# Performance work log

Hardware: AMD Instinct MI355X
Metric: run time of the kernel (lower is better)

Reference implementation:

```python
import jax, jax.numpy as jnp
import numpy as np

# dims
B, N, NF, NEF = 32, 256, 3, 3          # batch, nodes, node feats, edge feats
D, FF, H, L = 768, 3072, 12, 6         # embed, ffn, heads, layers
NA, ND, NE, NS = 512, 512, 512, 512    # vocab sizes (atoms, degrees, edges, spatial)
S = N + 1                              # +1 graph token
HD = D // H
SCALE = HD ** -0.5
EPS = 1e-5


def setup_inputs() -> dict:
    key = jax.random.key(0)
    ki = iter(jax.random.split(key, 64))
    def nrm(shape, std):
        return jax.random.normal(next(ki), shape, jnp.float32) * std
    lin_std = 0.02 / np.sqrt(L)
    inp = {}
    inp['x'] = jax.random.randint(next(ki), (B, N, NF), 0, NA)
    inp['attn_bias'] = jnp.zeros((B, S, S), jnp.float32)
    inp['spatial_pos'] = jax.random.randint(next(ki), (B, N, N), 0, NS)
    inp['attn_edge_type'] = jax.random.randint(next(ki), (B, N, N, NEF), 0, NE)
    inp['in_degree'] = jax.random.randint(next(ki), (B, N), 0, ND)
    inp['out_degree'] = jax.random.randint(next(ki), (B, N), 0, ND)
    # embedding tables (init_params overwrites padding rows with normals, so no zero row)
    inp['atom_emb'] = nrm((NA + 1, D), 0.02)
    inp['in_deg_emb'] = nrm((ND, D), 0.02)
    inp['out_deg_emb'] = nrm((ND, D), 0.02)
    inp['graph_token'] = nrm((1, D), 0.02)
    inp['spatial_emb'] = nrm((NS, H), 0.02)
    inp['edge_emb'] = nrm((NE + 1, H), 0.02)
    inp['virt_dist'] = nrm((1, H), 0.02)
    # stacked per-layer params (torch Linear convention: W is [out,in])
    for nm in ('Wq', 'Wk', 'Wv', 'Wo'):
        inp[nm] = nrm((L, D, D), lin_std)
    for nm in ('bq', 'bk', 'bv', 'bo'):
        inp[nm] = jnp.zeros((L, D), jnp.float32)
    inp['ln1_g'] = jnp.ones((L, D), jnp.float32); inp['ln1_b'] = jnp.zeros((L, D), jnp.float32)
    inp['ln2_g'] = jnp.ones((L, D), jnp.float32); inp['ln2_b'] = jnp.zeros((L, D), jnp.float32)
    inp['W1'] = nrm((L, FF, D), lin_std); inp['b1'] = jnp.zeros((L, FF), jnp.float32)
    inp['W2'] = nrm((L, D, FF), lin_std); inp['b2'] = jnp.zeros((L, D), jnp.float32)
    inp['fin_g'] = jnp.ones((D,), jnp.float32); inp['fin_b'] = jnp.zeros((D,), jnp.float32)
    return inp


def _ln(x, g, b):
    m = x.mean(-1, keepdims=True)
    v = jnp.mean((x - m) ** 2, axis=-1, keepdims=True)
    return (x - m) * jax.lax.rsqrt(v + EPS) * g + b


def _forward(x, attn_bias, spatial_pos, attn_edge_type, in_degree, out_degree, P):
    # --- GraphNodeFeature ---
    nf = P['atom_emb'][jnp.clip(x, 0, NA)].sum(-2)                     # [B,N,D]
    nf = nf + P['in_deg_emb'][jnp.clip(in_degree, 0, ND - 1)]
    nf = nf + P['out_deg_emb'][jnp.clip(out_degree, 0, ND - 1)]
    h = jnp.concatenate([jnp.broadcast_to(P['graph_token'][None], (B, 1, D)), nf], axis=1)  # [B,S,D]
    # --- GraphAttnBias ---
    inner = (P['spatial_emb'][jnp.clip(spatial_pos, 0, NS - 1)]
             + P['edge_emb'][jnp.clip(attn_edge_type, 0, NE)].mean(-2))  # [B,N,N,H]
    gb = jnp.broadcast_to(attn_bias[:, None], (B, H, S, S))
    gb = gb.at[:, :, 1:, 1:].add(jnp.transpose(inner, (0, 3, 1, 2)))
    t = P['virt_dist'].reshape(1, H, 1)
    gb = gb.at[:, :, 1:, 0].add(t)
    gb = gb.at[:, :, 0, :].add(t)
    # key padding mask: node is padded iff first feature index == 0; graph token never padded
    pad = jnp.concatenate([jnp.zeros((B, 1), bool), x[:, :, 0] == 0], axis=1)  # [B,S]
    maskk = pad[:, None, None, :]

    def step(hh, p):
        Wq, bq, Wk, bk, Wv, bv, Wo, bo, g1, bb_g1, W1, bf1, W2, bf2, g2, bb_g2 = p
        # pre-LN self-attention
        z = _ln(hh, g1, bb_g1)
        q = (jnp.einsum('bsi,oi->bso', z, Wq) + bq) * SCALE
        k = jnp.einsum('bsi,oi->bso', z, Wk) + bk
        v = jnp.einsum('bsi,oi->bso', z, Wv) + bv
        q = q.reshape(B, S, H, HD); k = k.reshape(B, S, H, HD); v = v.reshape(B, S, H, HD)
        scores = jnp.einsum('bqhd,bkhd->bhqk', q, k) + gb
        scores = jnp.where(maskk, -jnp.inf, scores)
        a = jax.nn.softmax(scores, axis=-1)
        o = jnp.einsum('bhqk,bkhd->bqhd', a, v).reshape(B, S, D)
        hh = hh + jnp.einsum('bsi,oi->bso', o, Wo) + bo
        # pre-LN FFN
        z = _ln(hh, g2, bb_g2)
        f = jax.nn.gelu(jnp.einsum('bsi,oi->bso', z, W1) + bf1, approximate=False)
        hh = hh + jnp.einsum('bsi,oi->bso', f, W2) + bf2
        return hh, None

    layer_params = (P['Wq'], P['bq'], P['Wk'], P['bk'], P['Wv'], P['bv'], P['Wo'], P['bo'],
                    P['ln1_g'], P['ln1_b'], P['W1'], P['b1'], P['W2'], P['b2'], P['ln2_g'], P['ln2_b'])
    h, _ = jax.lax.scan(step, h, layer_params)
    h = _ln(h, P['fin_g'], P['fin_b'])
    return h  # [B,S,D]


def reference(x, attn_bias, spatial_pos, attn_edge_type, in_degree, out_degree,
              atom_emb, in_deg_emb, out_deg_emb, graph_token, spatial_emb, edge_emb, virt_dist,
              Wq, Wk, Wv, Wo, bq, bk, bv, bo, ln1_g, ln1_b, ln2_g, ln2_b,
              W1, b1, W2, b2, fin_g, fin_b):
    P = dict(atom_emb=atom_emb, in_deg_emb=in_deg_emb, out_deg_emb=out_deg_emb,
             graph_token=graph_token, spatial_emb=spatial_emb, edge_emb=edge_emb, virt_dist=virt_dist,
             Wq=Wq, Wk=Wk, Wv=Wv, Wo=Wo, bq=bq, bk=bk, bv=bv, bo=bo,
             ln1_g=ln1_g, ln1_b=ln1_b, ln2_g=ln2_g, ln2_b=ln2_b,
             W1=W1, b1=b1, W2=W2, b2=b2, fin_g=fin_g, fin_b=fin_b)
    h = _forward(x, attn_bias, spatial_pos, attn_edge_type, in_degree, out_degree, P)
    node_rep = h[:, 1:, :]   # [B,N,D]
    graph_rep = h[:, 0, :]   # [B,D]
    return node_rep, graph_rep
```

## Files before the change

kernel.cpp:

```cpp
#include <hip/hip_runtime.h>
#include <hip/hip_bf16.h>
#include <math.h>

#define B_   32
#define N_   256
#define S_   257
#define D_   768
#define FF_  3072
#define H_   12
#define HD_  64
#define L_   6
#define NA_  512
#define ND_  512
#define NE_  512
#define NS_  512
#define SCALE_ 0.125f
#define EPS_ 1e-5f
#define NEG_BIG_ (-1e30f)

#define DD_  (D_ * D_)
#define FD_  (FF_ * D_)
#define WTOT_ (4 * DD_ + 2 * FD_)

typedef __hip_bfloat16 bf16;
typedef __attribute__((ext_vector_type(8))) short bf16x8;
typedef __attribute__((ext_vector_type(4))) float f32x4;

#define AS1 __attribute__((address_space(1)))
#define AS3 __attribute__((address_space(3)))

static __device__ __forceinline__ int iclamp(int v, int lo, int hi) {
    return v < lo ? lo : (v > hi ? hi : v);
}
static __device__ __forceinline__ float b2f(bf16 v) { return (float)v; }
static __device__ __forceinline__ short f2b(float f) {
    union { bf16 b; short s; } u; u.b = __float2bfloat16(f); return u.s;
}

__global__ __launch_bounds__(256) void embed_kernel(
    const int* __restrict__ x, const int* __restrict__ indeg,
    const int* __restrict__ outdeg, const float* __restrict__ atom_emb,
    const float* __restrict__ ine, const float* __restrict__ oute,
    const float* __restrict__ gtok, float* __restrict__ h)
{
    int row = blockIdx.x;
    int b = row / S_, s = row % S_;
    int t = threadIdx.x;
    float* hr = h + (size_t)row * D_;
    if (s == 0) {
        for (int d = t; d < D_; d += 256) hr[d] = gtok[d];
        return;
    }
    int n = s - 1;
    size_t xb = ((size_t)b * N_ + n) * 3;
    int i0 = iclamp(x[xb + 0], 0, NA_);
    int i1 = iclamp(x[xb + 1], 0, NA_);
    int i2 = iclamp(x[xb + 2], 0, NA_);
    int id = iclamp(indeg[(size_t)b * N_ + n], 0, ND_ - 1);
    int od = iclamp(outdeg[(size_t)b * N_ + n], 0, ND_ - 1);
    const float* a0 = atom_emb + (size_t)i0 * D_;
    const float* a1 = atom_emb + (size_t)i1 * D_;
    const float* a2 = atom_emb + (size_t)i2 * D_;
    const float* pi = ine + (size_t)id * D_;
    const float* po = oute + (size_t)od * D_;
    for (int d = t; d < D_; d += 256)
        hr[d] = a0[d] + a1[d] + a2[d] + pi[d] + po[d];
}

__global__ __launch_bounds__(256) void bias_kernel(
    const int* __restrict__ x, const float* __restrict__ ab,
    const int* __restrict__ sp, const int* __restrict__ et,
    const float* __restrict__ spemb, const float* __restrict__ eemb,
    const float* __restrict__ virt, bf16* __restrict__ bias)
{
    int row = blockIdx.x;
    int b = row / S_, q = row % S_;
    for (int k = threadIdx.x; k < S_; k += 256) {
        float abv = ab[((size_t)b * S_ + q) * S_ + k];
        bool masked = (k >= 1) && (x[((size_t)b * N_ + (k - 1)) * 3] == 0);
        size_t out_base = (size_t)b * H_ * S_ * S_ + (size_t)q * S_ + k;
        if (masked) {
            #pragma unroll
            for (int hh = 0; hh < H_; hh++)
                bias[out_base + (size_t)hh * S_ * S_] = __float2bfloat16(NEG_BIG_);
        } else if (q == 0 || k == 0) {
            #pragma unroll
            for (int hh = 0; hh < H_; hh++)
                bias[out_base + (size_t)hh * S_ * S_] = __float2bfloat16(abv + virt[hh]);
        } else {
            int spv = iclamp(sp[((size_t)b * N_ + (q - 1)) * N_ + (k - 1)], 0, NS_ - 1);
            size_t eb = (((size_t)b * N_ + (q - 1)) * N_ + (k - 1)) * 3;
            int e0 = iclamp(et[eb + 0], 0, NE_);
            int e1 = iclamp(et[eb + 1], 0, NE_);
            int e2 = iclamp(et[eb + 2], 0, NE_);
            #pragma unroll
            for (int hh = 0; hh < H_; hh++) {
                float inner = spemb[spv * H_ + hh]
                    + (eemb[e0 * H_ + hh] + eemb[e1 * H_ + hh] + eemb[e2 * H_ + hh]) * (1.0f / 3.0f);
                bias[out_base + (size_t)hh * S_ * S_] = __float2bfloat16(abv + inner);
            }
        }
    }
}

__global__ __launch_bounds__(256) void cvt_w_kernel(
    const float* __restrict__ Wq, const float* __restrict__ Wk,
    const float* __restrict__ Wv, const float* __restrict__ Wo,
    const float* __restrict__ W1, const float* __restrict__ W2,
    int layer, bf16* __restrict__ dst)
{
    size_t i = ((size_t)blockIdx.x * 256 + threadIdx.x) * 8;
    if (i >= (size_t)WTOT_) return;
    const float* src;
    if (i < (size_t)4 * DD_) {
        size_t r = i / DD_;
        const float* base = (r == 0) ? Wq : (r == 1) ? Wk : (r == 2) ? Wv : Wo;
        src = base + (size_t)layer * DD_ + (i - r * DD_);
    } else if (i < (size_t)4 * DD_ + FD_) {
        src = W1 + (size_t)layer * FD_ + (i - (size_t)4 * DD_);
    } else {
        src = W2 + (size_t)layer * FD_ + (i - (size_t)4 * DD_ - FD_);
    }
    float4 a = *(const float4*)src;
    float4 c = *(const float4*)(src + 4);
    *(bf16x8*)((short*)dst + i) =
        (bf16x8){f2b(a.x), f2b(a.y), f2b(a.z), f2b(a.w),
                 f2b(c.x), f2b(c.y), f2b(c.z), f2b(c.w)};
}

__global__ __launch_bounds__(256) void ln_kernel(
    const float* __restrict__ x, bf16* __restrict__ y,
    const float* __restrict__ g, const float* __restrict__ b)
{
    int row = blockIdx.x;
    int t = threadIdx.x;
    const float* xr = x + (size_t)row * D_;
    bf16* yr = y + (size_t)row * D_;
    float v0 = xr[t], v1 = xr[t + 256], v2 = xr[t + 512];
    __shared__ float rs[256], rq[256];
    rs[t] = v0 + v1 + v2;
    rq[t] = v0 * v0 + v1 * v1 + v2 * v2;
    __syncthreads();
    for (int o = 128; o > 0; o >>= 1) {
        if (t < o) { rs[t] += rs[t + o]; rq[t] += rq[t + o]; }
        __syncthreads();
    }
    float mean = rs[0] * (1.0f / D_);
    float var = fmaxf(rq[0] * (1.0f / D_) - mean * mean, 0.f);
    float inv = rsqrtf(var + EPS_);
    yr[t]       = __float2bfloat16((v0 - mean) * inv * g[t]       + b[t]);
    yr[t + 256] = __float2bfloat16((v1 - mean) * inv * g[t + 256] + b[t + 256]);
    yr[t + 512] = __float2bfloat16((v2 - mean) * inv * g[t + 512] + b[t + 512]);
}

__global__ __launch_bounds__(256) void final_ln_kernel(
    const float* __restrict__ x, const float* __restrict__ g,
    const float* __restrict__ b, float* __restrict__ out)
{
    int row = blockIdx.x;
    int bb = row / S_, s = row % S_;
    int t = threadIdx.x;
    const float* xr = x + (size_t)row * D_;
    float v0 = xr[t], v1 = xr[t + 256], v2 = xr[t + 512];
    __shared__ float rs[256], rq[256];
    rs[t] = v0 + v1 + v2;
    rq[t] = v0 * v0 + v1 * v1 + v2 * v2;
    __syncthreads();
    for (int o = 128; o > 0; o >>= 1) {
        if (t < o) { rs[t] += rs[t + o]; rq[t] += rq[t + o]; }
        __syncthreads();
    }
    float mean = rs[0] * (1.0f / D_);
    float var = fmaxf(rq[0] * (1.0f / D_) - mean * mean, 0.f);
    float inv = rsqrtf(var + EPS_);
    float* dst = (s == 0) ? out + (size_t)B_ * N_ * D_ + (size_t)bb * D_
                          : out + ((size_t)bb * N_ + (s - 1)) * D_;
    dst[t]       = (v0 - mean) * inv * g[t]       + b[t];
    dst[t + 256] = (v1 - mean) * inv * g[t + 256] + b[t + 256];
    dst[t + 512] = (v2 - mean) * inv * g[t + 512] + b[t + 512];
}

template <typename TC, int MODE>
__global__ __launch_bounds__(256) void mgemm(
    const bf16* __restrict__ A, const bf16* __restrict__ W,
    const float* __restrict__ bias, const float* __restrict__ res,
    TC* __restrict__ C, int M, int N, int K, float scale)
{
    __shared__ short As[128 * 32];
    __shared__ short Ws[128 * 32];
    AS3 short* AsL = (AS3 short*)As;
    AS3 short* WsL = (AS3 short*)Ws;
    const int t = threadIdx.x;
    const int lane = t & 63;
    const int w = t >> 6;
    const int wm = w & 1, wn = w >> 1;
    const int quad = lane >> 4;
    const int col = lane & 15;
    const int block_m = blockIdx.x * 128;
    const int block_n = blockIdx.y * 128;

    const int lrow = lane >> 2;
    const int lcol = (lane & 3) * 8;

    f32x4 acc[4][4];
    #pragma unroll
    for (int i = 0; i < 4; i++)
        #pragma unroll
        for (int j = 0; j < 4; j++)
            acc[i][j] = (f32x4){0.f, 0.f, 0.f, 0.f};

    for (int k0 = 0; k0 < K; k0 += 32) {
        #pragma unroll
        for (int ss = 0; ss < 2; ss++) {
            int seg = w * 2 + ss;
            int row = seg * 16 + lrow;
            const bf16* ga = A + (size_t)(block_m + row) * K + k0 + lcol;
            __builtin_amdgcn_global_load_lds((const AS1 void*)ga,
                                             (AS3 void*)(AsL + seg * 512), 16, 0, 0);
            const bf16* gw = W + (size_t)(block_n + row) * K + k0 + lcol;
            __builtin_amdgcn_global_load_lds((const AS1 void*)gw,
                                             (AS3 void*)(WsL + seg * 512), 16, 0, 0);
        }
        __syncthreads();
        bf16x8 af[4], bfr[4];
        #pragma unroll
        for (int mt = 0; mt < 4; mt++)
            af[mt] = *(const bf16x8*)&As[(wm * 64 + mt * 16 + col) * 32 + quad * 8];
        #pragma unroll
        for (int nt = 0; nt < 4; nt++)
            bfr[nt] = *(const bf16x8*)&Ws[(wn * 64 + nt * 16 + col) * 32 + quad * 8];
        #pragma unroll
        for (int mt = 0; mt < 4; mt++)
            #pragma unroll
            for (int nt = 0; nt < 4; nt++)
                acc[mt][nt] = __builtin_amdgcn_mfma_f32_16x16x32_bf16(
                    af[mt], bfr[nt], acc[mt][nt], 0, 0, 0);
        __syncthreads();
    }

    #pragma unroll
    for (int mt = 0; mt < 4; mt++) {
        #pragma unroll
        for (int nt = 0; nt < 4; nt++) {
            int gn = block_n + wn * 64 + nt * 16 + col;
            float bn = bias[gn];
            #pragma unroll
            for (int r = 0; r < 4; r++) {
                int gm = block_m + wm * 64 + mt * 16 + quad * 4 + r;
                if (gm < M) {
                    float val = acc[mt][nt][r] + bn;
                    if (MODE == 1) val *= scale;
                    if (MODE == 2) val = 0.5f * val * (1.0f + erff(val * 0.70710678118654752f));
                    if (MODE == 3) val += res[(size_t)gm * N + gn];
                    C[(size_t)gm * N + gn] = (TC)val;
                }
            }
        }
    }
}

__global__ __launch_bounds__(256) void attn_mfma(
    const bf16* __restrict__ qb, const bf16* __restrict__ kb,
    const bf16* __restrict__ vb, const bf16* __restrict__ bias,
    bf16* __restrict__ ob)
{
    __shared__ short Ks[64 * 72];
    __shared__ short Vt[64 * 72];
    __shared__ short Ps[4][16 * 72];

    const int t = threadIdx.x;
    const int lane = t & 63;
    const int wq = t >> 6;
    const int quad = lane >> 4;
    const int col = lane & 15;
    const int bh = blockIdx.y;
    const int hh = bh % H_;
    const int b = bh / H_;
    const int q0 = blockIdx.x * 64;

    bf16x8 qf[2];
    {
        int qrow = q0 + wq * 16 + col;
        #pragma unroll
        for (int kk = 0; kk < 2; kk++) {
            bf16x8 v = (bf16x8){0, 0, 0, 0, 0, 0, 0, 0};
            if (qrow < S_)
                v = *(const bf16x8*)(qb + ((size_t)(b * S_ + qrow)) * D_ + hh * HD_ + kk * 32 + quad * 8);
            qf[kk] = v;
        }
    }

    f32x4 o_acc[4];
    #pragma unroll
    for (int nt = 0; nt < 4; nt++) o_acc[nt] = (f32x4){0.f, 0.f, 0.f, 0.f};
    float m_run[4], l_run[4];
    #pragma unroll
    for (int r = 0; r < 4; r++) { m_run[r] = NEG_BIG_; l_run[r] = 0.f; }

    for (int kc = 0; kc < 5; kc++) {
        const int kbase = kc * 64;
        #pragma unroll
        for (int ss = 0; ss < 2; ss++) {
            int s = t + ss * 256;
            int row = s >> 3, dg = (s & 7) * 8;
            int gk = kbase + row;
            bf16x8 v = (bf16x8){0, 0, 0, 0, 0, 0, 0, 0};
            if (gk < S_)
                v = *(const bf16x8*)(kb + ((size_t)(b * S_ + gk)) * D_ + hh * HD_ + dg);
            *(bf16x8*)&Ks[row * 72 + dg] = v;
        }
        {
            int d = wq * 16 + col;
            const bf16* vcol = vb + ((size_t)(b * S_)) * D_ + hh * HD_ + d;
            #pragma unroll
            for (int ss = 0; ss < 8; ss++) {
                int kp = ss * 4 + quad;
                int gk = kbase + kp * 2;
                short v0 = (gk     < S_) ? *(const short*)(vcol + (size_t)gk * D_)       : (short)0;
                short v1 = (gk + 1 < S_) ? *(const short*)(vcol + (size_t)(gk + 1) * D_) : (short)0;
                unsigned pk = ((unsigned)(unsigned short)v0) |
                              ((unsigned)(unsigned short)v1 << 16);
                *(unsigned*)&Vt[d * 72 + kp * 2] = pk;
            }
        }
        __syncthreads();

        f32x4 s_acc[4];
        #pragma unroll
        for (int nt = 0; nt < 4; nt++) s_acc[nt] = (f32x4){0.f, 0.f, 0.f, 0.f};
        #pragma unroll
        for (int nt = 0; nt < 4; nt++) {
            #pragma unroll
            for (int kk = 0; kk < 2; kk++) {
                bf16x8 kfrag = *(const bf16x8*)&Ks[(nt * 16 + col) * 72 + kk * 32 + quad * 8];
                s_acc[nt] = __builtin_amdgcn_mfma_f32_16x16x32_bf16(qf[kk], kfrag, s_acc[nt], 0, 0, 0);
            }
        }

        const int qrow_base = q0 + wq * 16 + quad * 4;
        #pragma unroll
        for (int nt = 0; nt < 4; nt++) {
            int kglob = kbase + nt * 16 + col;
            #pragma unroll
            for (int r = 0; r < 4; r++) {
                int q = qrow_base + r;
                float sv = s_acc[nt][r];
                if (kglob >= S_)       sv = NEG_BIG_;
                else if (q < S_)       sv += b2f(bias[((size_t)bh * S_ + q) * S_ + kglob]);
                s_acc[nt][r] = sv;
            }
        }

        float alpha[4];
        #pragma unroll
        for (int r = 0; r < 4; r++) {
            float mx = fmaxf(fmaxf(s_acc[0][r], s_acc[1][r]),
                             fmaxf(s_acc[2][r], s_acc[3][r]));
            #pragma unroll
            for (int off = 8; off; off >>= 1) mx = fmaxf(mx, __shfl_xor(mx, off));
            float m_new = fmaxf(m_run[r], mx);
            alpha[r] = __expf(m_run[r] - m_new);
            m_run[r] = m_new;
            float ps = 0.f;
            #pragma unroll
            for (int nt = 0; nt < 4; nt++) {
                float p = __expf(s_acc[nt][r] - m_new);
                s_acc[nt][r] = p;
                ps += p;
            }
            #pragma unroll
            for (int off = 8; off; off >>= 1) ps += __shfl_xor(ps, off);
            l_run[r] = l_run[r] * alpha[r] + ps;
        }

        #pragma unroll
        for (int nt = 0; nt < 4; nt++)
            #pragma unroll
            for (int r = 0; r < 4; r++)
                Ps[wq][(quad * 4 + r) * 72 + nt * 16 + col] = f2b(s_acc[nt][r]);
        #pragma unroll
        for (int nt = 0; nt < 4; nt++)
            #pragma unroll
            for (int r = 0; r < 4; r++)
                o_acc[nt][r] *= alpha[r];

        bf16x8 pf[2];
        pf[0] = *(const bf16x8*)&Ps[wq][col * 72 + quad * 8];
        pf[1] = *(const bf16x8*)&Ps[wq][col * 72 + 32 + quad * 8];
        #pragma unroll
        for (int nt = 0; nt < 4; nt++) {
            #pragma unroll
            for (int kk = 0; kk < 2; kk++) {
                bf16x8 vfrag = *(const bf16x8*)&Vt[(nt * 16 + col) * 72 + kk * 32 + quad * 8];
                o_acc[nt] = __builtin_amdgcn_mfma_f32_16x16x32_bf16(pf[kk], vfrag, o_acc[nt], 0, 0, 0);
            }
        }
        __syncthreads();
    }

    const int qrow_base = q0 + wq * 16 + quad * 4;
    #pragma unroll
    for (int r = 0; r < 4; r++) {
        int q = qrow_base + r;
        if (q >= S_) continue;
        float invl = 1.0f / l_run[r];
        bf16* orow = ob + ((size_t)(b * S_ + q)) * D_ + hh * HD_;
        #pragma unroll
        for (int nt = 0; nt < 4; nt++)
            orow[nt * 16 + col] = __float2bfloat16(o_acc[nt][r] * invl);
    }
}

extern "C" void kernel_launch(void* const* d_in, const int* in_sizes, int n_in,
                              void* d_out, int out_size, void* d_ws, size_t ws_size,
                              hipStream_t stream)
{
    const int*   x         = (const int*)d_in[0];
    const float* attn_bias = (const float*)d_in[1];
    const int*   spatial   = (const int*)d_in[2];
    const int*   edget     = (const int*)d_in[3];
    const int*   indeg     = (const int*)d_in[4];
    const int*   outdeg    = (const int*)d_in[5];
    const float* atom_emb  = (const float*)d_in[6];
    const float* ine       = (const float*)d_in[7];
    const float* oute      = (const float*)d_in[8];
    const float* gtok      = (const float*)d_in[9];
    const float* spemb     = (const float*)d_in[10];
    const float* eemb      = (const float*)d_in[11];
    const float* virt      = (const float*)d_in[12];
    const float* Wq        = (const float*)d_in[13];
    const float* Wk        = (const float*)d_in[14];
    const float* Wv        = (const float*)d_in[15];
    const float* Wo        = (const float*)d_in[16];
    const float* bq        = (const float*)d_in[17];
    const float* bk        = (const float*)d_in[18];
    const float* bvv       = (const float*)d_in[19];
    const float* bo        = (const float*)d_in[20];
    const float* ln1g      = (const float*)d_in[21];
    const float* ln1b      = (const float*)d_in[22];
    const float* ln2g      = (const float*)d_in[23];
    const float* ln2b      = (const float*)d_in[24];
    const float* W1        = (const float*)d_in[25];
    const float* b1        = (const float*)d_in[26];
    const float* W2        = (const float*)d_in[27];
    const float* b2        = (const float*)d_in[28];
    const float* fing      = (const float*)d_in[29];
    const float* finb      = (const float*)d_in[30];

    const int M = B_ * S_;
    char* wsp = (char*)d_ws;
    size_t off = 0;
    auto alloc = [&](size_t bytes) -> void* {
        void* p = (void*)(wsp + off);
        off += (bytes + 255) & ~(size_t)255;
        return p;
    };
    float* h    = (float*)alloc((size_t)M * D_ * 4);
    bf16*  z    = (bf16*)alloc((size_t)M * D_ * 2);
    bf16*  qkv  = (bf16*)alloc((size_t)M * FF_ * 2);
    bf16*  bias = (bf16*)alloc((size_t)B_ * H_ * S_ * S_ * 2);
    bf16*  wbf  = (bf16*)alloc((size_t)WTOT_ * 2);
    bf16* qbuf = qkv;
    bf16* kbuf = qkv + (size_t)M * D_;
    bf16* vbuf = qkv + (size_t)2 * M * D_;
    bf16* fbuf = qkv;
    bf16* obuf = z;

    embed_kernel<<<M, 256, 0, stream>>>(x, indeg, outdeg, atom_emb, ine, oute, gtok, h);
    bias_kernel<<<M, 256, 0, stream>>>(x, attn_bias, spatial, edget, spemb, eemb, virt, bias);

    dim3 gD((M + 127) / 128, D_ / 128);
    dim3 gF((M + 127) / 128, FF_ / 128);
    dim3 gA(5, B_ * H_);
    const int cvtBlocks = WTOT_ / 2048;

    for (int l = 0; l < L_; l++) {
        cvt_w_kernel<<<cvtBlocks, 256, 0, stream>>>(Wq, Wk, Wv, Wo, W1, W2, l, wbf);
        ln_kernel<<<M, 256, 0, stream>>>(h, z, ln1g + l * D_, ln1b + l * D_);
        mgemm<bf16, 1><<<gD, 256, 0, stream>>>(z, wbf,            bq + l * D_, nullptr, qbuf, M, D_, D_, SCALE_);
        mgemm<bf16, 0><<<gD, 256, 0, stream>>>(z, wbf + DD_,      bk + l * D_, nullptr, kbuf, M, D_, D_, 1.f);
        mgemm<bf16, 0><<<gD, 256, 0, stream>>>(z, wbf + 2 * DD_,  bvv + l * D_, nullptr, vbuf, M, D_, D_, 1.f);
        attn_mfma<<<gA, 256, 0, stream>>>(qbuf, kbuf, vbuf, bias, obuf);
        mgemm<float, 3><<<gD, 256, 0, stream>>>(obuf, wbf + 3 * DD_, bo + l * D_, h, h, M, D_, D_, 1.f);
        ln_kernel<<<M, 256, 0, stream>>>(h, z, ln2g + l * D_, ln2b + l * D_);
        mgemm<bf16, 2><<<gF, 256, 0, stream>>>(z, wbf + 4 * DD_, b1 + l * FF_, nullptr, fbuf, M, FF_, D_, 1.f);
        mgemm<float, 3><<<gD, 256, 0, stream>>>(fbuf, wbf + 4 * DD_ + FD_, b2 + l * D_, h, h, M, D_, FF_, 1.f);
    }
    final_ln_kernel<<<M, 256, 0, stream>>>(h, fing, finb, (float*)d_out);
}
```

Before: 2.857 ms.

## Fuse QKV projections, double-buffer GEMM LDS, and remap workgroups across XCDs

```diff
diff --git a/kernel.cpp b/kernel.cpp
--- a/kernel.cpp
+++ b/kernel.cpp
@@ -21,6 +21,7 @@
 #define DD_  (D_ * D_)
 #define FD_  (FF_ * D_)
 #define WTOT_ (4 * DD_ + 2 * FD_)
+#define QKVN_ 2304
 
 typedef __hip_bfloat16 bf16;
 typedef __attribute__((ext_vector_type(8))) short bf16x8;
@@ -112,10 +113,12 @@
     size_t i = ((size_t)blockIdx.x * 256 + threadIdx.x) * 8;
     if (i >= (size_t)WTOT_) return;
     const float* src;
+    float sc = 1.f;
     if (i < (size_t)4 * DD_) {
         size_t r = i / DD_;
         const float* base = (r == 0) ? Wq : (r == 1) ? Wk : (r == 2) ? Wv : Wo;
         src = base + (size_t)layer * DD_ + (i - r * DD_);
+        if (r == 0) sc = SCALE_;
     } else if (i < (size_t)4 * DD_ + FD_) {
         src = W1 + (size_t)layer * FD_ + (i - (size_t)4 * DD_);
     } else {
@@ -124,8 +127,21 @@
     float4 a = *(const float4*)src;
     float4 c = *(const float4*)(src + 4);
     *(bf16x8*)((short*)dst + i) =
-        (bf16x8){f2b(a.x), f2b(a.y), f2b(a.z), f2b(a.w),
-                 f2b(c.x), f2b(c.y), f2b(c.z), f2b(c.w)};
+        (bf16x8){f2b(a.x * sc), f2b(a.y * sc), f2b(a.z * sc), f2b(a.w * sc),
+                 f2b(c.x * sc), f2b(c.y * sc), f2b(c.z * sc), f2b(c.w * sc)};
+}
+
+__global__ __launch_bounds__(256) void pack_bias_kernel(
+    const float* __restrict__ bq, const float* __restrict__ bk,
+    const float* __restrict__ bv, int layer, float* __restrict__ bqkv)
+{
+    int i = blockIdx.x * 256 + threadIdx.x;
+    if (i >= QKVN_) return;
+    float v;
+    if (i < D_)            v = bq[layer * D_ + i] * SCALE_;
+    else if (i < 2 * D_)   v = bk[layer * D_ + (i - D_)];
+    else                   v = bv[layer * D_ + (i - 2 * D_)];
+    bqkv[i] = v;
 }
 
 __global__ __launch_bounds__(256) void ln_kernel(
@@ -184,72 +200,85 @@
 __global__ __launch_bounds__(256) void mgemm(
     const bf16* __restrict__ A, const bf16* __restrict__ W,
     const float* __restrict__ bias, const float* __restrict__ res,
-    TC* __restrict__ C, int M, int N, int K, float scale)
-{
-    __shared__ short As[128 * 32];
-    __shared__ short Ws[128 * 32];
-    AS3 short* AsL = (AS3 short*)As;
-    AS3 short* WsL = (AS3 short*)Ws;
+    TC* __restrict__ C, int M, int N, int K, int gx)
+{
+    __shared__ short As[2][128 * 32];
+    __shared__ short Ws[2][128 * 32];
+    AS3 short* AsL = (AS3 short*)&As[0][0];
+    AS3 short* WsL = (AS3 short*)&Ws[0][0];
     const int t = threadIdx.x;
     const int lane = t & 63;
     const int w = t >> 6;
     const int wm = w & 1, wn = w >> 1;
     const int quad = lane >> 4;
     const int col = lane & 15;
-    const int block_m = blockIdx.x * 128;
-    const int block_n = blockIdx.y * 128;
+
+    const int nwg = gridDim.x;
+    const int orig = blockIdx.x;
+    const int q8 = nwg >> 3, r8 = nwg & 7;
+    const int xcd = orig & 7, li = orig >> 3;
+    const int wgid = (xcd < r8 ? xcd * (q8 + 1) : r8 * (q8 + 1) + (xcd - r8) * q8) + li;
+    const int block_m = (wgid % gx) * 128;
+    const int block_n = (wgid / gx) * 128;
 
     const int lrow = lane >> 2;
     const int lcol = (lane & 3) * 8;
 
-    f32x4 acc[4][4];
-    #pragma unroll
-    for (int i = 0; i < 4; i++)
-        #pragma unroll
-        for (int j = 0; j < 4; j++)
-            acc[i][j] = (f32x4){0.f, 0.f, 0.f, 0.f};
-
-    for (int k0 = 0; k0 < K; k0 += 32) {
+    auto stage = [&](int buf, int k0) {
         #pragma unroll
         for (int ss = 0; ss < 2; ss++) {
             int seg = w * 2 + ss;
             int row = seg * 16 + lrow;
             const bf16* ga = A + (size_t)(block_m + row) * K + k0 + lcol;
             __builtin_amdgcn_global_load_lds((const AS1 void*)ga,
-                                             (AS3 void*)(AsL + seg * 512), 16, 0, 0);
+                (AS3 void*)(AsL + buf * (128 * 32) + seg * 512), 16, 0, 0);
             const bf16* gw = W + (size_t)(block_n + row) * K + k0 + lcol;
             __builtin_amdgcn_global_load_lds((const AS1 void*)gw,
-                                             (AS3 void*)(WsL + seg * 512), 16, 0, 0);
-        }
+                (AS3 void*)(WsL + buf * (128 * 32) + seg * 512), 16, 0, 0);
+        }
+    };
+
+    f32x4 acc[4][4];
+    #pragma unroll
+    for (int i = 0; i < 4; i++)
+        #pragma unroll
+        for (int j = 0; j < 4; j++)
+            acc[i][j] = (f32x4){0.f, 0.f, 0.f, 0.f};
+
+    const int nt = K >> 5;
+    stage(0, 0);
+    __syncthreads();
+    int cur = 0;
+    for (int tt = 0; tt < nt; tt++) {
+        if (tt + 1 < nt) stage(cur ^ 1, (tt + 1) << 5);
+        bf16x8 af[4], bfr[4];
+        #pragma unroll
+        for (int mt = 0; mt < 4; mt++)
+            af[mt] = *(const bf16x8*)&As[cur][(wm * 64 + mt * 16 + col) * 32 + quad * 8];
+        #pragma unroll
+        for (int ntt = 0; ntt < 4; ntt++)
+            bfr[ntt] = *(const bf16x8*)&Ws[cur][(wn * 64 + ntt * 16 + col) * 32 + quad * 8];
+        #pragma unroll
+        for (int mt = 0; mt < 4; mt++)
+            #pragma unroll
+            for (int ntt = 0; ntt < 4; ntt++)
+                acc[mt][ntt] = __builtin_amdgcn_mfma_f32_16x16x32_bf16(
+                    af[mt], bfr[ntt], acc[mt][ntt], 0, 0, 0);
         __syncthreads();
-        bf16x8 af[4], bfr[4];
-        #pragma unroll
-        for (int mt = 0; mt < 4; mt++)
-            af[mt] = *(const bf16x8*)&As[(wm * 64 + mt * 16 + col) * 32 + quad * 8];
-        #pragma unroll
-        for (int nt = 0; nt < 4; nt++)
-            bfr[nt] = *(const bf16x8*)&Ws[(wn * 64 + nt * 16 + col) * 32 + quad * 8];
-        #pragma unroll
-        for (int mt = 0; mt < 4; mt++)
-            #pragma unroll
-            for (int nt = 0; nt < 4; nt++)
-                acc[mt][nt] = __builtin_amdgcn_mfma_f32_16x16x32_bf16(
-                    af[mt], bfr[nt], acc[mt][nt], 0, 0, 0);
-        __syncthreads();
+        cur ^= 1;
     }
 
     #pragma unroll
     for (int mt = 0; mt < 4; mt++) {
         #pragma unroll
-        for (int nt = 0; nt < 4; nt++) {
-            int gn = block_n + wn * 64 + nt * 16 + col;
+        for (int ntt = 0; ntt < 4; ntt++) {
+            int gn = block_n + wn * 64 + ntt * 16 + col;
             float bn = bias[gn];
             #pragma unroll
             for (int r = 0; r < 4; r++) {
                 int gm = block_m + wm * 64 + mt * 16 + quad * 4 + r;
                 if (gm < M) {
-                    float val = acc[mt][nt][r] + bn;
-                    if (MODE == 1) val *= scale;
+                    float val = acc[mt][ntt][r] + bn;
                     if (MODE == 2) val = 0.5f * val * (1.0f + erff(val * 0.70710678118654752f));
                     if (MODE == 3) val += res[(size_t)gm * N + gn];
                     C[(size_t)gm * N + gn] = (TC)val;
@@ -260,10 +289,12 @@
 }
 
 __global__ __launch_bounds__(256) void attn_mfma(
-    const bf16* __restrict__ qb, const bf16* __restrict__ kb,
-    const bf16* __restrict__ vb, const bf16* __restrict__ bias,
+    const bf16* __restrict__ qkv, const bf16* __restrict__ bias,
     bf16* __restrict__ ob)
 {
+    const bf16* qb = qkv;
+    const bf16* kb = qkv + D_;
+    const bf16* vb = qkv + 2 * D_;
     __shared__ short Ks[64 * 72];
     __shared__ short Vt[64 * 72];
     __shared__ short Ps[4][16 * 72];
@@ -285,7 +316,7 @@
         for (int kk = 0; kk < 2; kk++) {
             bf16x8 v = (bf16x8){0, 0, 0, 0, 0, 0, 0, 0};
             if (qrow < S_)
-                v = *(const bf16x8*)(qb + ((size_t)(b * S_ + qrow)) * D_ + hh * HD_ + kk * 32 + quad * 8);
+                v = *(const bf16x8*)(qb + ((size_t)(b * S_ + qrow)) * QKVN_ + hh * HD_ + kk * 32 + quad * 8);
             qf[kk] = v;
         }
     }
@@ -306,18 +337,18 @@
             int gk = kbase + row;
             bf16x8 v = (bf16x8){0, 0, 0, 0, 0, 0, 0, 0};
             if (gk < S_)
-                v = *(const bf16x8*)(kb + ((size_t)(b * S_ + gk)) * D_ + hh * HD_ + dg);
+                v = *(const bf16x8*)(kb + ((size_t)(b * S_ + gk)) * QKVN_ + hh * HD_ + dg);
             *(bf16x8*)&Ks[row * 72 + dg] = v;
         }
         {
             int d = wq * 16 + col;
-            const bf16* vcol = vb + ((size_t)(b * S_)) * D_ + hh * HD_ + d;
+            const bf16* vcol = vb + ((size_t)(b * S_)) * QKVN_ + hh * HD_ + d;
             #pragma unroll
             for (int ss = 0; ss < 8; ss++) {
                 int kp = ss * 4 + quad;
                 int gk = kbase + kp * 2;
-                short v0 = (gk     < S_) ? *(const short*)(vcol + (size_t)gk * D_)       : (short)0;
-                short v1 = (gk + 1 < S_) ? *(const short*)(vcol + (size_t)(gk + 1) * D_) : (short)0;
+                short v0 = (gk     < S_) ? *(const short*)(vcol + (size_t)gk * QKVN_)       : (short)0;
+                short v1 = (gk + 1 < S_) ? *(const short*)(vcol + (size_t)(gk + 1) * QKVN_) : (short)0;
                 unsigned pk = ((unsigned)(unsigned short)v0) |
                               ((unsigned)(unsigned short)v1 << 16);
                 *(unsigned*)&Vt[d * 72 + kp * 2] = pk;
@@ -460,31 +491,30 @@
     bf16*  qkv  = (bf16*)alloc((size_t)M * FF_ * 2);
     bf16*  bias = (bf16*)alloc((size_t)B_ * H_ * S_ * S_ * 2);
     bf16*  wbf  = (bf16*)alloc((size_t)WTOT_ * 2);
-    bf16* qbuf = qkv;
-    bf16* kbuf = qkv + (size_t)M * D_;
-    bf16* vbuf = qkv + (size_t)2 * M * D_;
+    float* bqkv = (float*)alloc((size_t)QKVN_ * 4);
     bf16* fbuf = qkv;
     bf16* obuf = z;
 
     embed_kernel<<<M, 256, 0, stream>>>(x, indeg, outdeg, atom_emb, ine, oute, gtok, h);
     bias_kernel<<<M, 256, 0, stream>>>(x, attn_bias, spatial, edget, spemb, eemb, virt, bias);
 
-    dim3 gD((M + 127) / 128, D_ / 128);
-    dim3 gF((M + 127) / 128, FF_ / 128);
+    const int gx = (M + 127) / 128;
+    const int nQKV = gx * (QKVN_ / 128);
+    const int nD   = gx * (D_ / 128);
+    const int nF   = gx * (FF_ / 128);
     dim3 gA(5, B_ * H_);
     const int cvtBlocks = WTOT_ / 2048;
 
     for (int l = 0; l < L_; l++) {
         cvt_w_kernel<<<cvtBlocks, 256, 0, stream>>>(Wq, Wk, Wv, Wo, W1, W2, l, wbf);
+        pack_bias_kernel<<<9, 256, 0, stream>>>(bq, bk, bvv, l, bqkv);
         ln_kernel<<<M, 256, 0, stream>>>(h, z, ln1g + l * D_, ln1b + l * D_);
-        mgemm<bf16, 1><<<gD, 256, 0, stream>>>(z, wbf,            bq + l * D_, nullptr, qbuf, M, D_, D_, SCALE_);
-        mgemm<bf16, 0><<<gD, 256, 0, stream>>>(z, wbf + DD_,      bk + l * D_, nullptr, kbuf, M, D_, D_, 1.f);
-        mgemm<bf16, 0><<<gD, 256, 0, stream>>>(z, wbf + 2 * DD_,  bvv + l * D_, nullptr, vbuf, M, D_, D_, 1.f);
-        attn_mfma<<<gA, 256, 0, stream>>>(qbuf, kbuf, vbuf, bias, obuf);
-        mgemm<float, 3><<<gD, 256, 0, stream>>>(obuf, wbf + 3 * DD_, bo + l * D_, h, h, M, D_, D_, 1.f);
+        mgemm<bf16, 0><<<nQKV, 256, 0, stream>>>(z, wbf, bqkv, nullptr, qkv, M, QKVN_, D_, gx);
+        attn_mfma<<<gA, 256, 0, stream>>>(qkv, bias, obuf);
+        mgemm<float, 3><<<nD, 256, 0, stream>>>(obuf, wbf + 3 * DD_, bo + l * D_, h, h, M, D_, D_, gx);
         ln_kernel<<<M, 256, 0, stream>>>(h, z, ln2g + l * D_, ln2b + l * D_);
-        mgemm<bf16, 2><<<gF, 256, 0, stream>>>(z, wbf + 4 * DD_, b1 + l * FF_, nullptr, fbuf, M, FF_, D_, 1.f);
-        mgemm<float, 3><<<gD, 256, 0, stream>>>(fbuf, wbf + 4 * DD_ + FD_, b2 + l * D_, h, h, M, D_, FF_, 1.f);
+        mgemm<bf16, 2><<<nF, 256, 0, stream>>>(z, wbf + 4 * DD_, b1 + l * FF_, nullptr, fbuf, M, FF_, D_, gx);
+        mgemm<float, 3><<<nD, 256, 0, stream>>>(fbuf, wbf + 4 * DD_ + FD_, b2 + l * D_, h, h, M, D_, FF_, gx);
     }
     final_ln_kernel<<<M, 256, 0, stream>>>(h, fing, finb, (float*)d_out);
 }
```

Result: faster. 2.562 ms (-10.3%).
